# Kernel optimization log

Measured on AMD Instinct MI355X. Metric: run time of the kernel, lower is better.

## Reference

```python
import jax, jax.numpy as jnp
import numpy as np

TEMP = 1.0


def _layernorm(x):
    # mean/std over last dim; torch.std is unbiased (ddof=1); no eps in original
    x = x - jnp.mean(x, axis=-1, keepdims=True)
    return x / jnp.std(x, axis=-1, keepdims=True, ddof=1)


def setup_inputs() -> dict:
    key = jax.random.key(0)
    ks = jax.random.split(key, 5)
    B, S, d_in, d = 8, 2048, 768, 1024
    return {
        "seq": jax.random.normal(ks[0], (B, S, d_in), dtype=jnp.float32),
        "embedding": jax.random.normal(ks[1], (d_in, d), dtype=jnp.float32),
        "W1": jax.random.normal(ks[2], (d, d), dtype=jnp.float32),
        "W2": jax.random.normal(ks[3], (d, d), dtype=jnp.float32),
        "readout": jax.random.normal(ks[4], (d,), dtype=jnp.float32),
    }


def reference(seq, embedding, W1, W2, readout):
    d_in = seq.shape[-1]
    d = embedding.shape[-1]
    x = jnp.matmul(seq, embedding) / jnp.sqrt(jnp.float32(d_in))  # [B,S,d]
    # depth == 1: single block
    gram = jnp.einsum("bsd,btd->bst", x, x) / x.shape[-1]  # [B,S,S]
    weights = jax.nn.softmax(gram / TEMP, axis=-1)
    post_attn = _layernorm(x + jnp.matmul(weights, x))  # [B,S,d]
    h = jnp.matmul(post_attn, W1) / jnp.sqrt(jnp.float32(d))
    h = jnp.matmul(jax.nn.relu(h), W2) / jnp.sqrt(jnp.float32(d))
    x = _layernorm(h + post_attn)
    pooled = jnp.mean(x, axis=1)  # [B,d]
    out = jnp.matmul(pooled, readout) / jnp.sqrt(jnp.float32(d))  # [B]
    return out
```

## Files before the change

kernel.cpp:

```cpp
#include <hip/hip_runtime.h>
#include <hip/hip_bf16.h>

typedef __bf16 bf16x8 __attribute__((ext_vector_type(8)));
typedef float f32x4 __attribute__((ext_vector_type(4)));

__device__ __forceinline__ unsigned short f2bf(float f) {
  union { float f; unsigned u; } x; x.f = f;
  unsigned r = x.u + 0x7fffu + ((x.u >> 16) & 1u);
  return (unsigned short)(r >> 16);
}
__device__ __forceinline__ float bf2f(unsigned short u) {
  union { unsigned u; float f; } x; x.u = (unsigned)u << 16;
  return x.f;
}
__device__ __forceinline__ unsigned short f2h(float f) {
  union { _Float16 h; unsigned short u; } x; x.h = (_Float16)f;
  return x.u;
}
__device__ __forceinline__ float h2f(unsigned short u) {
  union { _Float16 h; unsigned short u; } x; x.u = u;
  return (float)x.h;
}

__device__ __forceinline__ void async_ld16(const void* g, void* l) {
  __builtin_amdgcn_global_load_lds(
      (__attribute__((address_space(1))) void*)const_cast<void*>(g),
      (__attribute__((address_space(3))) void*)l, 16, 0, 0);
}


#define EPI_F32    0
#define EPI_BF     1
#define EPI_RELUBF 2
#define EPI_F16    3

__global__ __launch_bounds__(512, 2) void gemm_bt(
    const unsigned short* __restrict__ A,
    const unsigned short* __restrict__ Bt,
    int M, int N, int K, int nbatch,
    long sA, long sB, long sC,
    float scale, int mode, void* __restrict__ outp)
{
  __shared__ unsigned short lds[73728];
  const int t = threadIdx.x;
  const int w = t >> 6, l = t & 63;
  const int lr = l & 15, lg = l >> 4;
  const int wr = w >> 1, wc = w & 1;
  const int ntn = N >> 7;
  const int tiles = (M >> 8) * ntn;
  const int chunk = (tiles * nbatch) >> 3;
  const int bid = blockIdx.x;
  const int wg = (bid & 7) * chunk + (bid >> 3);
  const int batch = wg / tiles;
  const int rem = wg - batch * tiles;
  const int row0 = (rem / ntn) << 8;
  const int col0 = (rem % ntn) << 7;

  const unsigned short* Ab  = A  + (long)batch * sA;
  const unsigned short* Btb = Bt + (long)batch * sB;

  const int rsub = t >> 3;
  const int cg8  = ((t & 7) ^ (rsub & 7)) << 3;
  const long arow = (long)(row0 + rsub) * K;
  const long brow = (long)(col0 + rsub) * K;
  const long rstep = (long)K << 6;

  const int NT = K >> 6;

#define STAGE_A(buf, kk0)                                                   \
  {                                                                         \
    const unsigned short* s = Ab + arow + (kk0) + cg8;                      \
    unsigned short* d = (buf) + t * 8;                                      \
    async_ld16(s,             d);                                           \
    async_ld16(s + rstep,     d + 4096);                                    \
    async_ld16(s + 2 * rstep, d + 8192);                                    \
    async_ld16(s + 3 * rstep, d + 12288);                                   \
  }
#define STAGE_B(buf, kk0)                                                   \
  {                                                                         \
    const unsigned short* s = Btb + brow + (kk0) + cg8;                     \
    unsigned short* d = (buf) + 16384 + t * 8;                              \
    async_ld16(s,         d);                                               \
    async_ld16(s + rstep, d + 4096);                                        \
  }

  f32x4 acc[4][4];
#pragma unroll
  for (int m = 0; m < 4; ++m)
#pragma unroll
    for (int n = 0; n < 4; ++n) acc[m][n] = (f32x4){0.f, 0.f, 0.f, 0.f};

  STAGE_A(lds, 0); STAGE_B(lds, 0);
  STAGE_A(lds + 24576, 64); STAGE_B(lds + 24576, 64);
  asm volatile("s_waitcnt vmcnt(6)" ::: "memory");
  __builtin_amdgcn_s_barrier();
  __builtin_amdgcn_sched_barrier(0);

  for (int tt = 0; tt < NT; ++tt) {
    unsigned short* ldsA = lds + (tt % 3) * 24576;
    unsigned short* ldsB = ldsA + 16384;
    unsigned short* ldsN = lds + ((tt + 2) % 3) * 24576;
    const bool st = (tt + 2) < NT;
    const int kn = (tt + 2) << 6;

    if (st) STAGE_A(ldsN, kn);
    bf16x8 af[4][2], bfr[2][2];
#pragma unroll
    for (int mf = 0; mf < 4; ++mf) {
      int Ra = wr * 64 + mf * 16 + lr;
      int rb = Ra * 64, sw = (Ra & 7) << 3;
      af[mf][0] = *(const bf16x8*)&ldsA[rb + ((lg << 3) ^ sw)];
      af[mf][1] = *(const bf16x8*)&ldsA[rb + (((4 + lg) << 3) ^ sw)];
    }
#pragma unroll
    for (int n = 0; n < 2; ++n) {
      int Rb = wc * 64 + n * 16 + lr;
      int rb = Rb * 64, sw = (Rb & 7) << 3;
      bfr[n][0] = *(const bf16x8*)&ldsB[rb + ((lg << 3) ^ sw)];
      bfr[n][1] = *(const bf16x8*)&ldsB[rb + (((4 + lg) << 3) ^ sw)];
    }
    __builtin_amdgcn_sched_barrier(0);
    __builtin_amdgcn_s_barrier();
    __builtin_amdgcn_sched_barrier(0);
    __builtin_amdgcn_s_setprio(1);
#pragma unroll
    for (int kk = 0; kk < 2; ++kk)
#pragma unroll
      for (int mf = 0; mf < 4; ++mf)
#pragma unroll
        for (int n = 0; n < 2; ++n)
          acc[mf][n] = __builtin_amdgcn_mfma_f32_16x16x32_bf16(af[mf][kk], bfr[n][kk], acc[mf][n], 0, 0, 0);
    __builtin_amdgcn_s_setprio(0);
    __builtin_amdgcn_sched_barrier(0);
    __builtin_amdgcn_s_barrier();
    __builtin_amdgcn_sched_barrier(0);

    if (st) STAGE_B(ldsN, kn);
#pragma unroll
    for (int n = 0; n < 2; ++n) {
      int Rb = wc * 64 + (2 + n) * 16 + lr;
      int rb = Rb * 64, sw = (Rb & 7) << 3;
      bfr[n][0] = *(const bf16x8*)&ldsB[rb + ((lg << 3) ^ sw)];
      bfr[n][1] = *(const bf16x8*)&ldsB[rb + (((4 + lg) << 3) ^ sw)];
    }
    if (st) { asm volatile("s_waitcnt vmcnt(6)" ::: "memory"); }
    else    { asm volatile("s_waitcnt vmcnt(0)" ::: "memory"); }
    __builtin_amdgcn_sched_barrier(0);
    __builtin_amdgcn_s_barrier();
    __builtin_amdgcn_sched_barrier(0);
    __builtin_amdgcn_s_setprio(1);
#pragma unroll
    for (int kk = 0; kk < 2; ++kk)
#pragma unroll
      for (int mf = 0; mf < 4; ++mf)
#pragma unroll
        for (int n = 0; n < 2; ++n)
          acc[mf][2 + n] = __builtin_amdgcn_mfma_f32_16x16x32_bf16(af[mf][kk], bfr[n][kk], acc[mf][2 + n], 0, 0, 0);
    __builtin_amdgcn_s_setprio(0);
    __builtin_amdgcn_sched_barrier(0);
    __builtin_amdgcn_s_barrier();
    __builtin_amdgcn_sched_barrier(0);
  }

  float* outF = (float*)outp;
  unsigned short* outH = (unsigned short*)outp;
  const size_t cb = (size_t)batch * (size_t)sC;
#pragma unroll
  for (int mf = 0; mf < 4; ++mf) {
    int rbase = row0 + wr * 64 + mf * 16 + lg * 4;
#pragma unroll
    for (int nf = 0; nf < 4; ++nf) {
      int c = col0 + wc * 64 + nf * 16 + lr;
      f32x4 v = acc[mf][nf];
#pragma unroll
      for (int q = 0; q < 4; ++q) {
        size_t idx = cb + (size_t)(rbase + q) * N + c;
        float val = v[q] * scale;
        if (mode == EPI_F32)         outF[idx] = val;
        else if (mode == EPI_BF)     outH[idx] = f2bf(val);
        else if (mode == EPI_RELUBF) outH[idx] = f2bf(fmaxf(val, 0.f));
        else                         outH[idx] = f2h(val);
      }
    }
  }
#undef STAGE_A
#undef STAGE_B
}


__device__ __forceinline__ float wave_sum(float v) {
#pragma unroll
  for (int o = 32; o; o >>= 1) v += __shfl_xor(v, o, 64);
  return v;
}
__device__ __forceinline__ float wave_max(float v) {
#pragma unroll
  for (int o = 32; o; o >>= 1) v = fmaxf(v, __shfl_xor(v, o, 64));
  return v;
}

__global__ __launch_bounds__(256) void cast_bf16(const float* __restrict__ in,
                                                 unsigned short* __restrict__ out, long n) {
  long i = ((long)blockIdx.x * 256 + threadIdx.x) * 4;
  if (i >= n) return;
  float4 v = *(const float4*)&in[i];
  ushort4 o;
  o.x = f2bf(v.x); o.y = f2bf(v.y); o.z = f2bf(v.z); o.w = f2bf(v.w);
  *(ushort4*)&out[i] = o;
}

__global__ __launch_bounds__(256) void transpose_cast(const float* __restrict__ in,
                                                      unsigned short* __restrict__ out,
                                                      int R, int C) {
  __shared__ float tile[32][33];
  int c0 = blockIdx.x * 32, r0 = blockIdx.y * 32;
  int tx = threadIdx.x, ty = threadIdx.y;
  for (int i = ty; i < 32; i += 8) tile[i][tx] = in[(size_t)(r0 + i) * C + c0 + tx];
  __syncthreads();
  for (int i = ty; i < 32; i += 8) out[(size_t)(c0 + i) * R + r0 + tx] = f2bf(tile[tx][i]);
}

__global__ __launch_bounds__(256) void transpose_b16(const unsigned short* __restrict__ in,
                                                     unsigned short* __restrict__ out,
                                                     int R, int C) {
  __shared__ unsigned short tile[32][33];
  int c0 = blockIdx.x * 32, r0 = blockIdx.y * 32;
  size_t zb = (size_t)blockIdx.z * R * C;
  int tx = threadIdx.x, ty = threadIdx.y;
  for (int i = ty; i < 32; i += 8) tile[i][tx] = in[zb + (size_t)(r0 + i) * C + c0 + tx];
  __syncthreads();
  for (int i = ty; i < 32; i += 8) out[zb + (size_t)(c0 + i) * R + r0 + tx] = tile[tx][i];
}

__global__ __launch_bounds__(256) void softmax_rows(const unsigned short* __restrict__ g,
                                                    unsigned short* __restrict__ wout) {
  __shared__ float red[4];
  int row = blockIdx.x, t = threadIdx.x;
  const unsigned short* gr = g + ((size_t)row << 11) + t * 8;
  ushort4 ua = *(const ushort4*)gr;
  ushort4 ub = *(const ushort4*)(gr + 4);
  float a0 = h2f(ua.x), a1 = h2f(ua.y), a2 = h2f(ua.z), a3 = h2f(ua.w);
  float b0 = h2f(ub.x), b1 = h2f(ub.y), b2 = h2f(ub.z), b3 = h2f(ub.w);
  float mx = fmaxf(fmaxf(fmaxf(a0, a1), fmaxf(a2, a3)),
                   fmaxf(fmaxf(b0, b1), fmaxf(b2, b3)));
  mx = wave_max(mx);
  if ((t & 63) == 0) red[t >> 6] = mx;
  __syncthreads();
  mx = fmaxf(fmaxf(red[0], red[1]), fmaxf(red[2], red[3]));
  float e0 = __expf(a0 - mx), e1 = __expf(a1 - mx), e2 = __expf(a2 - mx), e3 = __expf(a3 - mx);
  float e4 = __expf(b0 - mx), e5 = __expf(b1 - mx), e6 = __expf(b2 - mx), e7 = __expf(b3 - mx);
  float s = ((e0 + e1) + (e2 + e3)) + ((e4 + e5) + (e6 + e7));
  s = wave_sum(s);
  __syncthreads();
  if ((t & 63) == 0) red[t >> 6] = s;
  __syncthreads();
  s = (red[0] + red[1]) + (red[2] + red[3]);
  float inv = 1.0f / s;
  ushort4 o0, o1;
  o0.x = f2bf(e0 * inv); o0.y = f2bf(e1 * inv); o0.z = f2bf(e2 * inv); o0.w = f2bf(e3 * inv);
  o1.x = f2bf(e4 * inv); o1.y = f2bf(e5 * inv); o1.z = f2bf(e6 * inv); o1.w = f2bf(e7 * inv);
  size_t base = ((size_t)row << 11) + t * 8;
  *(ushort4*)&wout[base] = o0;
  *(ushort4*)&wout[base + 4] = o1;
}

__global__ __launch_bounds__(256) void ln_residual_bf(const unsigned short* __restrict__ xb,
                                                      const float* __restrict__ attn,
                                                      unsigned short* __restrict__ outB) {
  __shared__ float red[4];
  int row = blockIdx.x, t = threadIdx.x;
  size_t base = ((size_t)row << 10) + t * 4;
  ushort4 ua = *(const ushort4*)&xb[base];
  float4 vb = *(const float4*)&attn[base];
  float4 v = {bf2f(ua.x) + vb.x, bf2f(ua.y) + vb.y, bf2f(ua.z) + vb.z, bf2f(ua.w) + vb.w};
  float s = (v.x + v.y) + (v.z + v.w);
  float ss = (v.x * v.x + v.y * v.y) + (v.z * v.z + v.w * v.w);
  s = wave_sum(s);
  if ((t & 63) == 0) red[t >> 6] = s;
  __syncthreads();
  s = (red[0] + red[1]) + (red[2] + red[3]);
  ss = wave_sum(ss);
  __syncthreads();
  if ((t & 63) == 0) red[t >> 6] = ss;
  __syncthreads();
  ss = (red[0] + red[1]) + (red[2] + red[3]);
  float mean = s * (1.0f / 1024.0f);
  float var = (ss - s * mean) * (1.0f / 1023.0f);
  float rstd = rsqrtf(var);
  ushort4 ob;
  ob.x = f2bf((v.x - mean) * rstd); ob.y = f2bf((v.y - mean) * rstd);
  ob.z = f2bf((v.z - mean) * rstd); ob.w = f2bf((v.w - mean) * rstd);
  *(ushort4*)&outB[base] = ob;
}

__global__ __launch_bounds__(256) void ln_residual_dot(const unsigned short* __restrict__ h2,
                                                       const unsigned short* __restrict__ post,
                                                       const float* __restrict__ readout,
                                                       float* __restrict__ rowdot) {
  __shared__ float red[4];
  int row = blockIdx.x, t = threadIdx.x;
  size_t base = ((size_t)row << 10) + t * 4;
  ushort4 ua = *(const ushort4*)&h2[base];
  ushort4 ub = *(const ushort4*)&post[base];
  float4 v = {bf2f(ua.x) + bf2f(ub.x), bf2f(ua.y) + bf2f(ub.y),
              bf2f(ua.z) + bf2f(ub.z), bf2f(ua.w) + bf2f(ub.w)};
  float s = (v.x + v.y) + (v.z + v.w);
  float ss = (v.x * v.x + v.y * v.y) + (v.z * v.z + v.w * v.w);
  s = wave_sum(s);
  if ((t & 63) == 0) red[t >> 6] = s;
  __syncthreads();
  s = (red[0] + red[1]) + (red[2] + red[3]);
  ss = wave_sum(ss);
  __syncthreads();
  if ((t & 63) == 0) red[t >> 6] = ss;
  __syncthreads();
  ss = (red[0] + red[1]) + (red[2] + red[3]);
  float mean = s * (1.0f / 1024.0f);
  float var = (ss - s * mean) * (1.0f / 1023.0f);
  float rstd = rsqrtf(var);
  float4 r = *(const float4*)&readout[t * 4];
  float dot = (v.x - mean) * rstd * r.x + (v.y - mean) * rstd * r.y +
              (v.z - mean) * rstd * r.z + (v.w - mean) * rstd * r.w;
  dot = wave_sum(dot);
  __syncthreads();
  if ((t & 63) == 0) red[t >> 6] = dot;
  __syncthreads();
  if (t == 0) rowdot[row] = (red[0] + red[1]) + (red[2] + red[3]);
}

__global__ __launch_bounds__(256) void reduce_out(const float* __restrict__ rowdot,
                                                  float* __restrict__ out) {
  __shared__ float red[4];
  int b = blockIdx.x, t = threadIdx.x;
  float s = 0.f;
  for (int i = t; i < 2048; i += 256) s += rowdot[(size_t)b * 2048 + i];
  s = wave_sum(s);
  if ((t & 63) == 0) red[t >> 6] = s;
  __syncthreads();
  if (t == 0) out[b] = ((red[0] + red[1]) + (red[2] + red[3])) * (1.0f / 65536.0f);
}

extern "C" void kernel_launch(void* const* d_in, const int* in_sizes, int n_in,
                              void* d_out, int out_size, void* d_ws, size_t ws_size,
                              hipStream_t stream) {
  const float* seq     = (const float*)d_in[0];
  const float* emb     = (const float*)d_in[1];
  const float* W1      = (const float*)d_in[2];
  const float* W2      = (const float*)d_in[3];
  const float* readout = (const float*)d_in[4];
  float* out = (float*)d_out;

  char* ws = (char*)d_ws;
  const size_t MB = 1024u * 1024u;
  unsigned short* x_b    = (unsigned short*)(ws + 0);
  unsigned short* h2b    = (unsigned short*)(ws + 0);
  unsigned short* xT     = (unsigned short*)(ws + 32 * MB);
  unsigned short* hrelu  = (unsigned short*)(ws + 32 * MB);
  unsigned short* gram   = (unsigned short*)(ws + 64 * MB);
  float*          attn   = (float*)(ws + 64 * MB);
  unsigned short* wts    = (unsigned short*)(ws + 128 * MB);
  unsigned short* post_b = (unsigned short*)(ws + 128 * MB);
  unsigned short* seq_b  = (unsigned short*)(ws + 192 * MB);
  unsigned short* embT   = (unsigned short*)(ws + 216 * MB);
  unsigned short* W1T    = (unsigned short*)(ws + 218 * MB);
  unsigned short* W2T    = (unsigned short*)(ws + 220 * MB);
  float*          rowdot = (float*)(ws + 222 * MB);

  cast_bf16<<<12288, 256, 0, stream>>>(seq, seq_b, 12582912L);
  transpose_cast<<<dim3(32, 24), dim3(32, 8), 0, stream>>>(emb, embT, 768, 1024);
  transpose_cast<<<dim3(32, 32), dim3(32, 8), 0, stream>>>(W1, W1T, 1024, 1024);
  transpose_cast<<<dim3(32, 32), dim3(32, 8), 0, stream>>>(W2, W2T, 1024, 1024);

  gemm_bt<<<512, 512, 0, stream>>>(seq_b, embT, 16384, 1024, 768, 1, 0, 0, 0,
                                   0.03608439182435161f, EPI_BF, x_b);

  transpose_b16<<<dim3(32, 64, 8), dim3(32, 8), 0, stream>>>(x_b, xT, 2048, 1024);

  gemm_bt<<<1024, 512, 0, stream>>>(x_b, x_b, 2048, 2048, 1024, 8,
                                    2048L * 1024, 2048L * 1024, 2048L * 2048,
                                    1.0f / 1024.0f, EPI_F16, gram);

  softmax_rows<<<16384, 256, 0, stream>>>(gram, wts);

  gemm_bt<<<512, 512, 0, stream>>>(wts, xT, 2048, 1024, 2048, 8,
                                   2048L * 2048, 1024L * 2048, 2048L * 1024,
                                   1.0f, EPI_F32, attn);

  ln_residual_bf<<<16384, 256, 0, stream>>>(x_b, attn, post_b);

  gemm_bt<<<512, 512, 0, stream>>>(post_b, W1T, 16384, 1024, 1024, 1, 0, 0, 0,
                                   0.03125f, EPI_RELUBF, hrelu);
  gemm_bt<<<512, 512, 0, stream>>>(hrelu, W2T, 16384, 1024, 1024, 1, 0, 0, 0,
                                   0.03125f, EPI_BF, h2b);

  ln_residual_dot<<<16384, 256, 0, stream>>>(h2b, post_b, readout, rowdot);
  reduce_out<<<8, 256, 0, stream>>>(rowdot, out);
}
```

Before: 430.5 us.

## Enlarge GEMM tile to 256x256 with double-buffered single-stage pipeline

```diff
diff --git a/kernel.cpp b/kernel.cpp
--- a/kernel.cpp
+++ b/kernel.cpp
@@ -41,12 +41,12 @@
     long sA, long sB, long sC,
     float scale, int mode, void* __restrict__ outp)
 {
-  __shared__ unsigned short lds[73728];
+  __shared__ unsigned short lds[65536];
   const int t = threadIdx.x;
   const int w = t >> 6, l = t & 63;
   const int lr = l & 15, lg = l >> 4;
-  const int wr = w >> 1, wc = w & 1;
-  const int ntn = N >> 7;
+  const int wr = w >> 2, wc = w & 3;
+  const int ntn = N >> 8;
   const int tiles = (M >> 8) * ntn;
   const int chunk = (tiles * nbatch) >> 3;
   const int bid = blockIdx.x;
@@ -54,7 +54,7 @@
   const int batch = wg / tiles;
   const int rem = wg - batch * tiles;
   const int row0 = (rem / ntn) << 8;
-  const int col0 = (rem % ntn) << 7;
+  const int col0 = (rem % ntn) << 8;
 
   const unsigned short* Ab  = A  + (long)batch * sA;
   const unsigned short* Btb = Bt + (long)batch * sB;
@@ -67,98 +67,70 @@
 
   const int NT = K >> 6;
 
-#define STAGE_A(buf, kk0)                                                   \
+#define STAGE(buf, kk0)                                                     \
   {                                                                         \
-    const unsigned short* s = Ab + arow + (kk0) + cg8;                      \
-    unsigned short* d = (buf) + t * 8;                                      \
-    async_ld16(s,             d);                                           \
-    async_ld16(s + rstep,     d + 4096);                                    \
-    async_ld16(s + 2 * rstep, d + 8192);                                    \
-    async_ld16(s + 3 * rstep, d + 12288);                                   \
+    const unsigned short* sa = Ab + arow + (kk0) + cg8;                     \
+    const unsigned short* sb = Btb + brow + (kk0) + cg8;                    \
+    unsigned short* da = (buf) + t * 8;                                     \
+    unsigned short* db = (buf) + 16384 + t * 8;                             \
+    async_ld16(sa,             da);                                         \
+    async_ld16(sa + rstep,     da + 4096);                                  \
+    async_ld16(sa + 2 * rstep, da + 8192);                                  \
+    async_ld16(sa + 3 * rstep, da + 12288);                                 \
+    async_ld16(sb,             db);                                         \
+    async_ld16(sb + rstep,     db + 4096);                                  \
+    async_ld16(sb + 2 * rstep, db + 8192);                                  \
+    async_ld16(sb + 3 * rstep, db + 12288);                                 \
   }
-#define STAGE_B(buf, kk0)                                                   \
-  {                                                                         \
-    const unsigned short* s = Btb + brow + (kk0) + cg8;                     \
-    unsigned short* d = (buf) + 16384 + t * 8;                              \
-    async_ld16(s,         d);                                               \
-    async_ld16(s + rstep, d + 4096);                                        \
-  }
-
-  f32x4 acc[4][4];
-#pragma unroll
-  for (int m = 0; m < 4; ++m)
+
+  f32x4 acc[8][4];
+#pragma unroll
+  for (int m = 0; m < 8; ++m)
 #pragma unroll
     for (int n = 0; n < 4; ++n) acc[m][n] = (f32x4){0.f, 0.f, 0.f, 0.f};
 
-  STAGE_A(lds, 0); STAGE_B(lds, 0);
-  STAGE_A(lds + 24576, 64); STAGE_B(lds + 24576, 64);
-  asm volatile("s_waitcnt vmcnt(6)" ::: "memory");
-  __builtin_amdgcn_s_barrier();
+  STAGE(lds, 0);
   __builtin_amdgcn_sched_barrier(0);
 
   for (int tt = 0; tt < NT; ++tt) {
-    unsigned short* ldsA = lds + (tt % 3) * 24576;
+    unsigned short* ldsA = lds + (tt & 1) * 32768;
     unsigned short* ldsB = ldsA + 16384;
-    unsigned short* ldsN = lds + ((tt + 2) % 3) * 24576;
-    const bool st = (tt + 2) < NT;
-    const int kn = (tt + 2) << 6;
-
-    if (st) STAGE_A(ldsN, kn);
-    bf16x8 af[4][2], bfr[2][2];
-#pragma unroll
-    for (int mf = 0; mf < 4; ++mf) {
-      int Ra = wr * 64 + mf * 16 + lr;
-      int rb = Ra * 64, sw = (Ra & 7) << 3;
-      af[mf][0] = *(const bf16x8*)&ldsA[rb + ((lg << 3) ^ sw)];
-      af[mf][1] = *(const bf16x8*)&ldsA[rb + (((4 + lg) << 3) ^ sw)];
-    }
-#pragma unroll
-    for (int n = 0; n < 2; ++n) {
-      int Rb = wc * 64 + n * 16 + lr;
-      int rb = Rb * 64, sw = (Rb & 7) << 3;
-      bfr[n][0] = *(const bf16x8*)&ldsB[rb + ((lg << 3) ^ sw)];
-      bfr[n][1] = *(const bf16x8*)&ldsB[rb + (((4 + lg) << 3) ^ sw)];
+    unsigned short* ldsN = lds + ((tt + 1) & 1) * 32768;
+
+    __builtin_amdgcn_s_barrier();
+    __builtin_amdgcn_sched_barrier(0);
+    if (tt + 1 < NT) {
+      STAGE(ldsN, (tt + 1) << 6);
+      __builtin_amdgcn_sched_barrier(0);
+      asm volatile("s_waitcnt vmcnt(8)" ::: "memory");
+    } else {
+      asm volatile("s_waitcnt vmcnt(0)" ::: "memory");
     }
     __builtin_amdgcn_sched_barrier(0);
     __builtin_amdgcn_s_barrier();
     __builtin_amdgcn_sched_barrier(0);
-    __builtin_amdgcn_s_setprio(1);
-#pragma unroll
-    for (int kk = 0; kk < 2; ++kk)
-#pragma unroll
-      for (int mf = 0; mf < 4; ++mf)
-#pragma unroll
-        for (int n = 0; n < 2; ++n)
-          acc[mf][n] = __builtin_amdgcn_mfma_f32_16x16x32_bf16(af[mf][kk], bfr[n][kk], acc[mf][n], 0, 0, 0);
-    __builtin_amdgcn_s_setprio(0);
-    __builtin_amdgcn_sched_barrier(0);
-    __builtin_amdgcn_s_barrier();
-    __builtin_amdgcn_sched_barrier(0);
-
-    if (st) STAGE_B(ldsN, kn);
-#pragma unroll
-    for (int n = 0; n < 2; ++n) {
-      int Rb = wc * 64 + (2 + n) * 16 + lr;
-      int rb = Rb * 64, sw = (Rb & 7) << 3;
-      bfr[n][0] = *(const bf16x8*)&ldsB[rb + ((lg << 3) ^ sw)];
-      bfr[n][1] = *(const bf16x8*)&ldsB[rb + (((4 + lg) << 3) ^ sw)];
+
+#pragma unroll
+    for (int kk = 0; kk < 2; ++kk) {
+      bf16x8 af[8], bfr[4];
+#pragma unroll
+      for (int mf = 0; mf < 8; ++mf) {
+        int Ra = wr * 128 + mf * 16 + lr;
+        af[mf] = *(const bf16x8*)&ldsA[Ra * 64 + ((kk * 32 + lg * 8) ^ ((Ra & 7) << 3))];
+      }
+#pragma unroll
+      for (int nf = 0; nf < 4; ++nf) {
+        int Rb = wc * 64 + nf * 16 + lr;
+        bfr[nf] = *(const bf16x8*)&ldsB[Rb * 64 + ((kk * 32 + lg * 8) ^ ((Rb & 7) << 3))];
+      }
+      __builtin_amdgcn_s_setprio(1);
+#pragma unroll
+      for (int mf = 0; mf < 8; ++mf)
+#pragma unroll
+        for (int nf = 0; nf < 4; ++nf)
+          acc[mf][nf] = __builtin_amdgcn_mfma_f32_16x16x32_bf16(af[mf], bfr[nf], acc[mf][nf], 0, 0, 0);
+      __builtin_amdgcn_s_setprio(0);
     }
-    if (st) { asm volatile("s_waitcnt vmcnt(6)" ::: "memory"); }
-    else    { asm volatile("s_waitcnt vmcnt(0)" ::: "memory"); }
-    __builtin_amdgcn_sched_barrier(0);
-    __builtin_amdgcn_s_barrier();
-    __builtin_amdgcn_sched_barrier(0);
-    __builtin_amdgcn_s_setprio(1);
-#pragma unroll
-    for (int kk = 0; kk < 2; ++kk)
-#pragma unroll
-      for (int mf = 0; mf < 4; ++mf)
-#pragma unroll
-        for (int n = 0; n < 2; ++n)
-          acc[mf][2 + n] = __builtin_amdgcn_mfma_f32_16x16x32_bf16(af[mf][kk], bfr[n][kk], acc[mf][2 + n], 0, 0, 0);
-    __builtin_amdgcn_s_setprio(0);
-    __builtin_amdgcn_sched_barrier(0);
-    __builtin_amdgcn_s_barrier();
     __builtin_amdgcn_sched_barrier(0);
   }
 
@@ -166,8 +138,8 @@
   unsigned short* outH = (unsigned short*)outp;
   const size_t cb = (size_t)batch * (size_t)sC;
 #pragma unroll
-  for (int mf = 0; mf < 4; ++mf) {
-    int rbase = row0 + wr * 64 + mf * 16 + lg * 4;
+  for (int mf = 0; mf < 8; ++mf) {
+    int rbase = row0 + wr * 128 + mf * 16 + lg * 4;
 #pragma unroll
     for (int nf = 0; nf < 4; ++nf) {
       int c = col0 + wc * 64 + nf * 16 + lr;
@@ -183,8 +155,7 @@
       }
     }
   }
-#undef STAGE_A
-#undef STAGE_B
+#undef STAGE
 }
 
 
@@ -371,26 +342,26 @@
   transpose_cast<<<dim3(32, 32), dim3(32, 8), 0, stream>>>(W1, W1T, 1024, 1024);
   transpose_cast<<<dim3(32, 32), dim3(32, 8), 0, stream>>>(W2, W2T, 1024, 1024);
 
-  gemm_bt<<<512, 512, 0, stream>>>(seq_b, embT, 16384, 1024, 768, 1, 0, 0, 0,
+  gemm_bt<<<256, 512, 0, stream>>>(seq_b, embT, 16384, 1024, 768, 1, 0, 0, 0,
                                    0.03608439182435161f, EPI_BF, x_b);
 
   transpose_b16<<<dim3(32, 64, 8), dim3(32, 8), 0, stream>>>(x_b, xT, 2048, 1024);
 
-  gemm_bt<<<1024, 512, 0, stream>>>(x_b, x_b, 2048, 2048, 1024, 8,
-                                    2048L * 1024, 2048L * 1024, 2048L * 2048,
-                                    1.0f / 1024.0f, EPI_F16, gram);
+  gemm_bt<<<512, 512, 0, stream>>>(x_b, x_b, 2048, 2048, 1024, 8,
+                                   2048L * 1024, 2048L * 1024, 2048L * 2048,
+                                   1.0f / 1024.0f, EPI_F16, gram);
 
   softmax_rows<<<16384, 256, 0, stream>>>(gram, wts);
 
-  gemm_bt<<<512, 512, 0, stream>>>(wts, xT, 2048, 1024, 2048, 8,
+  gemm_bt<<<256, 512, 0, stream>>>(wts, xT, 2048, 1024, 2048, 8,
                                    2048L * 2048, 1024L * 2048, 2048L * 1024,
                                    1.0f, EPI_F32, attn);
 
   ln_residual_bf<<<16384, 256, 0, stream>>>(x_b, attn, post_b);
 
-  gemm_bt<<<512, 512, 0, stream>>>(post_b, W1T, 16384, 1024, 1024, 1, 0, 0, 0,
+  gemm_bt<<<256, 512, 0, stream>>>(post_b, W1T, 16384, 1024, 1024, 1, 0, 0, 0,
                                    0.03125f, EPI_RELUBF, hrelu);
-  gemm_bt<<<512, 512, 0, stream>>>(hrelu, W2T, 16384, 1024, 1024, 1, 0, 0, 0,
+  gemm_bt<<<256, 512, 0, stream>>>(hrelu, W2T, 16384, 1024, 1024, 1, 0, 0, 0,
                                    0.03125f, EPI_BF, h2b);
 
   ln_residual_dot<<<16384, 256, 0, stream>>>(h2b, post_b, readout, rowdot);
```

Result: faster. 393.9 us (-8.5%).
